# Performance work log

Hardware: AMD Instinct MI355X
Metric: run time of the kernel (lower is better)

The kernel has to match this reference:

```python
import jax, jax.numpy as jnp
import numpy as np

EPS = 1e-8  # torch F.cosine_similarity clamps norms at eps=1e-8


def setup_inputs() -> dict:
    key = jax.random.key(0)
    N, M, D = 1024, 20, 768  # speakers, utterances/speaker, embed dim
    embeddings = jax.random.normal(key, (N, M, D), dtype=jnp.float32)
    w = jnp.asarray(10.0, dtype=jnp.float32)  # init_w
    b = jnp.asarray(-5.0, dtype=jnp.float32)  # init_b
    return {"embeddings": embeddings, "w": w, "b": b}


def reference(embeddings, w, b):
    N, M, D = embeddings.shape
    centroids = embeddings.mean(axis=1)  # [N, D]
    # cosine similarity as one fused GEMM on normalized vectors
    e = embeddings / jnp.maximum(
        jnp.linalg.norm(embeddings, axis=-1, keepdims=True), EPS)
    c = centroids / jnp.maximum(
        jnp.linalg.norm(centroids, axis=-1, keepdims=True), EPS)
    # sim[j, i, m] = cos(e[i, m], centroid[j])  -- matches the torch loop/stack
    sim = jnp.einsum('imd,jd->jim', e, c)
    logits = w * sim + b  # [N_j, N_i, M]
    # torch: view(N*N, M).transpose(0,1).reshape(-1, N)
    #   => row index r = m*N + j, column i
    logits = jnp.transpose(logits, (2, 0, 1)).reshape(N * M, N)
    # torch labels: arange(N) expanded over M -> labels[r] = r // M
    labels = jnp.repeat(jnp.arange(N), M)
    logp = jax.nn.log_softmax(logits, axis=-1)
    loss = -jnp.mean(logp[jnp.arange(N * M), labels])
    return loss
```

## Files before the change

### kernel.cpp

```cpp
#include <hip/hip_runtime.h>
#include <hip/hip_bf16.h>
#include <cstdint>

#define N_SPK 1024
#define M_UTT 20
#define D_DIM 768
#define NM_ROWS (N_SPK * M_UTT)

static constexpr float EPS = 1e-8f;

#define WAIT_VM0   0x0F70
#define WAIT_VM8   0x0F78
#define WAIT_LGKM0 0xC07F

typedef __attribute__((ext_vector_type(4))) float floatx4;
typedef __attribute__((ext_vector_type(4))) int   intx4;
typedef __attribute__((ext_vector_type(8))) int   intx8;

__device__ __forceinline__ void load16_to_lds(const void* g, void* l) {
    __builtin_amdgcn_global_load_lds(
        (const __attribute__((address_space(1))) uint32_t*)g,
        (__attribute__((address_space(3))) uint32_t*)l, 16, 0, 0);
}

__device__ __forceinline__ float wave_sum(float v) {
    #pragma unroll
    for (int o = 32; o > 0; o >>= 1) v += __shfl_xor(v, o);
    return v;
}

__device__ __forceinline__ unsigned short fp8pk(float a, float b) {
    return (unsigned short)(__builtin_amdgcn_cvt_pk_fp8_f32(a, b, 0, false) & 0xFFFF);
}

__device__ __forceinline__ int kperm(int d) {
    return (d & ~63) | (((d >> 3) & 3) << 4) | (((d >> 5) & 1) << 3) | (d & 7);
}

__global__ __launch_bounds__(384) void prep_kernel(const float* __restrict__ emb,
                                                   unsigned char* __restrict__ ehat,
                                                   unsigned char* __restrict__ chat,
                                                   int* __restrict__ ctr,
                                                   float* __restrict__ accum) {
    const int i = blockIdx.x;
    const int t = threadIdx.x;
    const int wave = t >> 6, lane = t & 63;

    if (i == 0 && t == 0) { *ctr = 0; *accum = 0.f; }

    const float2* src = (const float2*)(emb + (size_t)i * M_UTT * D_DIM);
    const int dp = kperm(t * 2);

    float2 v[M_UTT];
    float ss[M_UTT];
    float2 cen = {0.f, 0.f};
    #pragma unroll
    for (int m = 0; m < M_UTT; ++m) {
        const float2 x = src[m * 384 + t];
        v[m] = x;
        ss[m] = x.x * x.x + x.y * x.y;
        cen.x += x.x; cen.y += x.y;
    }
    cen.x *= (1.f / M_UTT); cen.y *= (1.f / M_UTT);
    float css = cen.x * cen.x + cen.y * cen.y;

    __shared__ float red[M_UTT + 1][6];
    #pragma unroll
    for (int m = 0; m < M_UTT; ++m) {
        const float s = wave_sum(ss[m]);
        if (lane == 0) red[m][wave] = s;
    }
    {
        const float s = wave_sum(css);
        if (lane == 0) red[M_UTT][wave] = s;
    }
    __syncthreads();

    #pragma unroll
    for (int m = 0; m < M_UTT; ++m) {
        const float tot = red[m][0] + red[m][1] + red[m][2] +
                          red[m][3] + red[m][4] + red[m][5];
        const float rn = 1.0f / fmaxf(sqrtf(tot), EPS);
        *(unsigned short*)(ehat + ((size_t)(m * N_SPK + i)) * D_DIM + dp) =
            fp8pk(v[m].x * rn, v[m].y * rn);
    }
    {
        const float tot = red[M_UTT][0] + red[M_UTT][1] + red[M_UTT][2] +
                          red[M_UTT][3] + red[M_UTT][4] + red[M_UTT][5];
        const float rn = 1.0f / fmaxf(sqrtf(tot), EPS);
        *(unsigned short*)(chat + (size_t)i * D_DIM + dp) =
            fp8pk(cen.x * rn, cen.y * rn);
    }
}

__global__ __launch_bounds__(256, 2) void gemm_fused_kernel(
        const unsigned char* __restrict__ ehat,
        const unsigned char* __restrict__ chat,
        const float* __restrict__ wp,
        float* __restrict__ Psum,
        float* __restrict__ T) {
    __shared__ unsigned char As[2][128 * 128];
    __shared__ unsigned char Bs[2][128 * 128];

    const int t    = threadIdx.x;
    const int lane = t & 63;
    const int c    = lane & 15;
    const int quad = lane >> 4;
    const int wid  = t >> 6;
    const int wr   = wid >> 1;
    const int wc   = wid & 1;

    const int xcd = blockIdx.x & 7;
    const int idx = blockIdx.x >> 3;
    const int bu  = xcd * 20 + (idx >> 3);
    const int bj  = idx & 7;
    const int m   = bu >> 3;
    const int rb8 = bu & 7;
    const int u0  = bu * 128;
    const int j0  = bj * 128;

    const unsigned char* Ag = ehat + (size_t)u0 * D_DIM;
    const unsigned char* Bg = chat + (size_t)j0 * D_DIM;

    int goff[4];
    int boffB[4], bdst[4];
    #pragma unroll
    for (int s = 0; s < 4; ++s) {
        const int ci  = s * 256 + t;
        const int row = ci >> 3;
        goff[s]  = row * D_DIM + (((ci & 7) ^ (row & 7)) * 16);
        boffB[s] = row * D_DIM + ((ci & 7) * 16);
        bdst[s]  = row * 128 + (((ci & 7) ^ (row & 7)) * 16);
    }

    int slotA[4], slotB[4];
    #pragma unroll
    for (int f = 0; f < 4; ++f) {
        const int rA = wr * 64 + f * 16 + c;
        const int rB = wc * 64 + f * 16 + c;
        slotA[f] = rA * 128 + ((quad ^ (c & 7)) * 16);
        slotB[f] = rB * 128 + ((quad ^ (c & 7)) * 16);
    }

    floatx4 acc[4][4] = {};
    intx4 breg[4];

    #pragma unroll
    for (int s = 0; s < 4; ++s)
        load16_to_lds(Ag + goff[s], &As[0][(s * 256 + t) * 16]);
    intx4 b0[4], b1[4];
    #pragma unroll
    for (int s = 0; s < 4; ++s) b0[s] = *(const intx4*)(Bg + boffB[s]);
    #pragma unroll
    for (int s = 0; s < 4; ++s) b1[s] = *(const intx4*)(Bg + boffB[s] + 128);
    #pragma unroll
    for (int s = 0; s < 4; ++s)
        load16_to_lds(Ag + goff[s] + 128, &As[1][(s * 256 + t) * 16]);
    #pragma unroll
    for (int s = 0; s < 4; ++s) *(intx4*)(&Bs[0][bdst[s]]) = b0[s];
    #pragma unroll
    for (int s = 0; s < 4; ++s) *(intx4*)(&Bs[1][bdst[s]]) = b1[s];
    #pragma unroll
    for (int s = 0; s < 4; ++s) breg[s] = *(const intx4*)(Bg + boffB[s] + 256);
    __builtin_amdgcn_s_waitcnt(WAIT_LGKM0);
    __builtin_amdgcn_sched_barrier(0);
    __builtin_amdgcn_s_barrier();
    __builtin_amdgcn_sched_barrier(0);

    #pragma unroll
    for (int kt = 0; kt < 6; ++kt) {
        const int cur = kt & 1;

        if (kt > 0) {
            if (kt < 5) __builtin_amdgcn_s_waitcnt(WAIT_VM8);
            else        __builtin_amdgcn_s_waitcnt(WAIT_VM0);
            __builtin_amdgcn_s_waitcnt(WAIT_LGKM0);
            __builtin_amdgcn_sched_barrier(0);
            __builtin_amdgcn_s_barrier();
            __builtin_amdgcn_sched_barrier(0);
        }

        intx8 av[4], bv[4];
        #pragma unroll
        for (int f = 0; f < 4; ++f) {
            const intx4 lo = *(const intx4*)(&As[cur][slotA[f]]);
            const intx4 hi = *(const intx4*)(&As[cur][slotA[f] ^ 64]);
            av[f] = __builtin_shufflevector(lo, hi, 0, 1, 2, 3, 4, 5, 6, 7);
        }
        #pragma unroll
        for (int f = 0; f < 4; ++f) {
            const intx4 lo = *(const intx4*)(&Bs[cur][slotB[f]]);
            const intx4 hi = *(const intx4*)(&Bs[cur][slotB[f] ^ 64]);
            bv[f] = __builtin_shufflevector(lo, hi, 0, 1, 2, 3, 4, 5, 6, 7);
        }

        __builtin_amdgcn_s_setprio(1);
        #pragma unroll
        for (int it = 0; it < 4; ++it)
            #pragma unroll
            for (int jt = 0; jt < 4; ++jt)
                acc[it][jt] = __builtin_amdgcn_mfma_scale_f32_16x16x128_f8f6f4(
                    av[it], bv[jt], acc[it][jt],
                    0, 0,
                    0, 0x7F7F7F7F,
                    0, 0x7F7F7F7F);
        __builtin_amdgcn_s_setprio(0);

        if (kt < 4) {
            __builtin_amdgcn_s_waitcnt(WAIT_LGKM0);
            __builtin_amdgcn_sched_barrier(0);
            __builtin_amdgcn_s_barrier();
            __builtin_amdgcn_sched_barrier(0);
            const int k0 = (kt + 2) * 128;
            #pragma unroll
            for (int s = 0; s < 4; ++s)
                load16_to_lds(Ag + goff[s] + k0, &As[cur][(s * 256 + t) * 16]);
            #pragma unroll
            for (int s = 0; s < 4; ++s) *(intx4*)(&Bs[cur][bdst[s]]) = breg[s];
            if (kt < 3) {
                const int k1 = (kt + 3) * 128;
                #pragma unroll
                for (int s = 0; s < 4; ++s)
                    breg[s] = *(const intx4*)(Bg + boffB[s] + k1);
            }
            __builtin_amdgcn_sched_barrier(0);
        }
    }

    const float w = wp[0];
    const int rb320 = bu * 2 + wr;

    #pragma unroll
    for (int jt = 0; jt < 4; ++jt) {
        float sm = 0.f;
        #pragma unroll
        for (int it = 0; it < 4; ++it)
            #pragma unroll
            for (int r = 0; r < 4; ++r)
                sm += __expf(w * (acc[it][jt][r] - 1.0f));
        sm += __shfl_xor(sm, 16);
        sm += __shfl_xor(sm, 32);
        if (quad == 0)
            Psum[(size_t)rb320 * N_SPK + j0 + wc * 64 + jt * 16 + c] = sm;
    }

    #pragma unroll
    for (int it = 0; it < 4; ++it) {
        #pragma unroll
        for (int jt = 0; jt < 4; ++jt) {
            const int col = j0 + wc * 64 + jt * 16 + c;
            const int g = m * N_SPK + col;
            const int istar = g / M_UTT;
            const int rloc = rb8 * 128 + wr * 64 + it * 16 + quad * 4;
            #pragma unroll
            for (int r = 0; r < 4; ++r) {
                if (rloc + r == istar) T[g] = acc[it][jt][r];
            }
        }
    }
}

__global__ void combine_kernel(const float* __restrict__ Psum,
                               const float* __restrict__ T,
                               const float* __restrict__ wp,
                               int* __restrict__ ctr,
                               float* __restrict__ accum,
                               float* __restrict__ out) {
    const int p = blockIdx.x * 256 + threadIdx.x;
    const int m = p >> 10;
    const int j = p & 1023;
    const float w = wp[0];

    float S = 0.f;
    #pragma unroll
    for (int rb = 0; rb < 16; ++rb)
        S += Psum[(size_t)(m * 16 + rb) * N_SPK + j];
    const float term = w * (T[p] - 1.0f) - __logf(S);

    __shared__ float red[256];
    red[threadIdx.x] = term;
    __syncthreads();
    for (int o = 128; o > 0; o >>= 1) {
        if (threadIdx.x < o) red[threadIdx.x] += red[threadIdx.x + o];
        __syncthreads();
    }
    if (threadIdx.x == 0) {
        atomicAdd(accum, red[0]);
        __threadfence();
        const int old = atomicAdd(ctr, 1);
        if (old == 79) {
            const float a = atomicAdd(accum, 0.0f);
            out[0] = -a / (float)NM_ROWS;
        }
    }
}

extern "C" void kernel_launch(void* const* d_in, const int* in_sizes, int n_in,
                              void* d_out, int out_size, void* d_ws, size_t ws_size,
                              hipStream_t stream) {
    const float* emb = (const float*)d_in[0];
    const float* wp  = (const float*)d_in[1];
    float* out = (float*)d_out;

    char* ws = (char*)d_ws;
    unsigned char* ehat = (unsigned char*)(ws);
    unsigned char* chat = (unsigned char*)(ws + 15728640);
    float* Psum  = (float*)(ws + 16515072);
    float* T     = (float*)(ws + 17825792);
    int*   ctr   = (int*)  (ws + 17907712);
    float* accum = (float*)(ws + 17907716);

    prep_kernel<<<dim3(N_SPK), dim3(384), 0, stream>>>(emb, ehat, chat, ctr, accum);
    gemm_fused_kernel<<<dim3(1280), dim3(256), 0, stream>>>(ehat, chat, wp, Psum, T);
    combine_kernel<<<dim3(80), dim3(256), 0, stream>>>(Psum, T, wp, ctr, accum, out);
}
```

Before: 130.3 us.

## Widen GEMM tile to 128x256 with single-buffered B and register prefetch

Doubles the per-block N tile from 128 to 256 centroid columns, halving the grid to 640 blocks. Each wave now holds a 4x8 accumulator set. B is stored in a single LDS buffer refilled from register prefetch, while A keeps double buffering. The aim is more reuse of each A tile and fewer redundant A loads across blocks, at the cost of more registers and lower occupancy or parallelism with only 640 blocks.

New measurement: 210.4 us. +61.4%, slower.

```diff
diff --git a/kernel.cpp b/kernel.cpp
--- a/kernel.cpp
+++ b/kernel.cpp
@@ -10,7 +10,7 @@
 static constexpr float EPS = 1e-8f;
 
 #define WAIT_VM0   0x0F70
-#define WAIT_VM8   0x0F78
+#define WAIT_VM12  0x0F7C
 #define WAIT_LGKM0 0xC07F
 
 typedef __attribute__((ext_vector_type(4))) float floatx4;
@@ -100,7 +100,7 @@
         float* __restrict__ Psum,
         float* __restrict__ T) {
     __shared__ unsigned char As[2][128 * 128];
-    __shared__ unsigned char Bs[2][128 * 128];
+    __shared__ unsigned char Bs[256 * 128];
 
     const int t    = threadIdx.x;
     const int lane = t & 63;
@@ -112,56 +112,43 @@
 
     const int xcd = blockIdx.x & 7;
     const int idx = blockIdx.x >> 3;
-    const int bu  = xcd * 20 + (idx >> 3);
-    const int bj  = idx & 7;
+    const int bu  = xcd * 20 + (idx >> 2);
+    const int bj  = idx & 3;
     const int m   = bu >> 3;
     const int rb8 = bu & 7;
     const int u0  = bu * 128;
-    const int j0  = bj * 128;
+    const int j0  = bj * 256;
 
     const unsigned char* Ag = ehat + (size_t)u0 * D_DIM;
     const unsigned char* Bg = chat + (size_t)j0 * D_DIM;
 
-    int goff[4];
-    int boffB[4], bdst[4];
-    #pragma unroll
-    for (int s = 0; s < 4; ++s) {
-        const int ci  = s * 256 + t;
-        const int row = ci >> 3;
-        goff[s]  = row * D_DIM + (((ci & 7) ^ (row & 7)) * 16);
-        boffB[s] = row * D_DIM + ((ci & 7) * 16);
-        bdst[s]  = row * 128 + (((ci & 7) ^ (row & 7)) * 16);
-    }
-
-    int slotA[4], slotB[4];
-    #pragma unroll
-    for (int f = 0; f < 4; ++f) {
-        const int rA = wr * 64 + f * 16 + c;
-        const int rB = wc * 64 + f * 16 + c;
-        slotA[f] = rA * 128 + ((quad ^ (c & 7)) * 16);
-        slotB[f] = rB * 128 + ((quad ^ (c & 7)) * 16);
-    }
-
-    floatx4 acc[4][4] = {};
-    intx4 breg[4];
+    const int row0  = t >> 3;
+    const int goff0 = row0 * D_DIM + (((t & 7) ^ (row0 & 7)) * 16);
+    const int boff0 = row0 * D_DIM + ((t & 7) * 16);
+    const int bdst0 = row0 * 128 + (((t & 7) ^ (row0 & 7)) * 16);
+
+    const int sw     = (quad ^ (c & 7)) * 16;
+    const int slotA0 = (wr * 64 + c) * 128 + sw;
+    const int slotB0 = (wc * 128 + c) * 128 + sw;
+
+    floatx4 acc[4][8] = {};
+    intx4 breg[8];
 
     #pragma unroll
     for (int s = 0; s < 4; ++s)
-        load16_to_lds(Ag + goff[s], &As[0][(s * 256 + t) * 16]);
-    intx4 b0[4], b1[4];
-    #pragma unroll
-    for (int s = 0; s < 4; ++s) b0[s] = *(const intx4*)(Bg + boffB[s]);
-    #pragma unroll
-    for (int s = 0; s < 4; ++s) b1[s] = *(const intx4*)(Bg + boffB[s] + 128);
+        load16_to_lds(Ag + goff0 + s * 32 * D_DIM,       &As[0][(s * 256 + t) * 16]);
     #pragma unroll
     for (int s = 0; s < 4; ++s)
-        load16_to_lds(Ag + goff[s] + 128, &As[1][(s * 256 + t) * 16]);
-    #pragma unroll
-    for (int s = 0; s < 4; ++s) *(intx4*)(&Bs[0][bdst[s]]) = b0[s];
-    #pragma unroll
-    for (int s = 0; s < 4; ++s) *(intx4*)(&Bs[1][bdst[s]]) = b1[s];
-    #pragma unroll
-    for (int s = 0; s < 4; ++s) breg[s] = *(const intx4*)(Bg + boffB[s] + 256);
+        load16_to_lds(Ag + goff0 + s * 32 * D_DIM + 128, &As[1][(s * 256 + t) * 16]);
+    #pragma unroll
+    for (int s = 0; s < 8; ++s)
+        breg[s] = *(const intx4*)(Bg + boff0 + s * 32 * D_DIM);
+    #pragma unroll
+    for (int s = 0; s < 8; ++s)
+        *(intx4*)(&Bs[bdst0 + s * 32 * 128]) = breg[s];
+    #pragma unroll
+    for (int s = 0; s < 8; ++s)
+        breg[s] = *(const intx4*)(Bg + boff0 + s * 32 * D_DIM + 128);
     __builtin_amdgcn_s_waitcnt(WAIT_LGKM0);
     __builtin_amdgcn_sched_barrier(0);
     __builtin_amdgcn_s_barrier();
@@ -172,7 +159,7 @@
         const int cur = kt & 1;
 
         if (kt > 0) {
-            if (kt < 5) __builtin_amdgcn_s_waitcnt(WAIT_VM8);
+            if (kt < 5) __builtin_amdgcn_s_waitcnt(WAIT_VM12);
             else        __builtin_amdgcn_s_waitcnt(WAIT_VM0);
             __builtin_amdgcn_s_waitcnt(WAIT_LGKM0);
             __builtin_amdgcn_sched_barrier(0);
@@ -180,48 +167,56 @@
             __builtin_amdgcn_sched_barrier(0);
         }
 
-        intx8 av[4], bv[4];
+        intx8 av[4];
         #pragma unroll
         for (int f = 0; f < 4; ++f) {
-            const intx4 lo = *(const intx4*)(&As[cur][slotA[f]]);
-            const intx4 hi = *(const intx4*)(&As[cur][slotA[f] ^ 64]);
+            const int sa = slotA0 + f * 2048;
+            const intx4 lo = *(const intx4*)(&As[cur][sa]);
+            const intx4 hi = *(const intx4*)(&As[cur][sa ^ 64]);
             av[f] = __builtin_shufflevector(lo, hi, 0, 1, 2, 3, 4, 5, 6, 7);
         }
         #pragma unroll
-        for (int f = 0; f < 4; ++f) {
-            const intx4 lo = *(const intx4*)(&Bs[cur][slotB[f]]);
-            const intx4 hi = *(const intx4*)(&Bs[cur][slotB[f] ^ 64]);
-            bv[f] = __builtin_shufflevector(lo, hi, 0, 1, 2, 3, 4, 5, 6, 7);
-        }
-
-        __builtin_amdgcn_s_setprio(1);
-        #pragma unroll
-        for (int it = 0; it < 4; ++it)
-            #pragma unroll
-            for (int jt = 0; jt < 4; ++jt)
-                acc[it][jt] = __builtin_amdgcn_mfma_scale_f32_16x16x128_f8f6f4(
-                    av[it], bv[jt], acc[it][jt],
-                    0, 0,
-                    0, 0x7F7F7F7F,
-                    0, 0x7F7F7F7F);
-        __builtin_amdgcn_s_setprio(0);
-
-        if (kt < 4) {
+        for (int g = 0; g < 2; ++g) {
+            intx8 bv[4];
+            #pragma unroll
+            for (int j = 0; j < 4; ++j) {
+                const int sb = slotB0 + (g * 4 + j) * 2048;
+                const intx4 lo = *(const intx4*)(&Bs[sb]);
+                const intx4 hi = *(const intx4*)(&Bs[sb ^ 64]);
+                bv[j] = __builtin_shufflevector(lo, hi, 0, 1, 2, 3, 4, 5, 6, 7);
+            }
+            __builtin_amdgcn_s_setprio(1);
+            #pragma unroll
+            for (int it = 0; it < 4; ++it)
+                #pragma unroll
+                for (int j = 0; j < 4; ++j)
+                    acc[it][g * 4 + j] = __builtin_amdgcn_mfma_scale_f32_16x16x128_f8f6f4(
+                        av[it], bv[j], acc[it][g * 4 + j],
+                        0, 0,
+                        0, 0x7F7F7F7F,
+                        0, 0x7F7F7F7F);
+            __builtin_amdgcn_s_setprio(0);
+        }
+
+        if (kt < 5) {
             __builtin_amdgcn_s_waitcnt(WAIT_LGKM0);
             __builtin_amdgcn_sched_barrier(0);
             __builtin_amdgcn_s_barrier();
             __builtin_amdgcn_sched_barrier(0);
             const int k0 = (kt + 2) * 128;
-            #pragma unroll
-            for (int s = 0; s < 4; ++s)
-                load16_to_lds(Ag + goff[s] + k0, &As[cur][(s * 256 + t) * 16]);
-            #pragma unroll
-            for (int s = 0; s < 4; ++s) *(intx4*)(&Bs[cur][bdst[s]]) = breg[s];
-            if (kt < 3) {
-                const int k1 = (kt + 3) * 128;
+            if (kt < 4) {
                 #pragma unroll
                 for (int s = 0; s < 4; ++s)
-                    breg[s] = *(const intx4*)(Bg + boffB[s] + k1);
+                    load16_to_lds(Ag + goff0 + s * 32 * D_DIM + k0,
+                                  &As[cur][(s * 256 + t) * 16]);
+            }
+            #pragma unroll
+            for (int s = 0; s < 8; ++s)
+                *(intx4*)(&Bs[bdst0 + s * 32 * 128]) = breg[s];
+            if (kt < 4) {
+                #pragma unroll
+                for (int s = 0; s < 8; ++s)
+                    breg[s] = *(const intx4*)(Bg + boff0 + s * 32 * D_DIM + k0);
             }
             __builtin_amdgcn_sched_barrier(0);
         }
@@ -231,7 +226,7 @@
     const int rb320 = bu * 2 + wr;
 
     #pragma unroll
-    for (int jt = 0; jt < 4; ++jt) {
+    for (int jt = 0; jt < 8; ++jt) {
         float sm = 0.f;
         #pragma unroll
         for (int it = 0; it < 4; ++it)
@@ -241,14 +236,14 @@
         sm += __shfl_xor(sm, 16);
         sm += __shfl_xor(sm, 32);
         if (quad == 0)
-            Psum[(size_t)rb320 * N_SPK + j0 + wc * 64 + jt * 16 + c] = sm;
+            Psum[(size_t)rb320 * N_SPK + j0 + wc * 128 + jt * 16 + c] = sm;
     }
 
     #pragma unroll
     for (int it = 0; it < 4; ++it) {
         #pragma unroll
-        for (int jt = 0; jt < 4; ++jt) {
-            const int col = j0 + wc * 64 + jt * 16 + c;
+        for (int jt = 0; jt < 8; ++jt) {
+            const int col = j0 + wc * 128 + jt * 16 + c;
             const int g = m * N_SPK + col;
             const int istar = g / M_UTT;
             const int rloc = rb8 * 128 + wr * 64 + it * 16 + quad * 4;
@@ -311,6 +306,6 @@
     float* accum = (float*)(ws + 17907716);
 
     prep_kernel<<<dim3(N_SPK), dim3(384), 0, stream>>>(emb, ehat, chat, ctr, accum);
-    gemm_fused_kernel<<<dim3(1280), dim3(256), 0, stream>>>(ehat, chat, wp, Psum, T);
+    gemm_fused_kernel<<<dim3(640), dim3(256), 0, stream>>>(ehat, chat, wp, Psum, T);
     combine_kernel<<<dim3(80), dim3(256), 0, stream>>>(Psum, T, wp, ctr, accum, out);
 }
```
